# Kernel optimization log

Hardware: AMD Instinct MI355X
Metric: run time of the kernel (lower is better)

## Reference

```python
import jax, jax.numpy as jnp
import numpy as np

B, TX, TY, D, H = 8, 128, 128, 512, 512
LN_EPS = 1e-3  # keras LayerNormalization default epsilon


def setup_inputs() -> dict:
    key = jax.random.key(0)
    ks = jax.random.split(key, 6)
    scale = 1.0 / np.sqrt(D)
    return {
        "context": jax.random.normal(ks[0], (B, TX, D), jnp.float32),
        "x": jax.random.normal(ks[1], (B, TY, D), jnp.float32),
        "Wa": jax.random.normal(ks[2], (D, H), jnp.float32) * scale,
        "bWa": jnp.zeros((H,), jnp.float32),
        "Ua": jax.random.normal(ks[3], (D, H), jnp.float32) * scale,
        "bUa": jnp.zeros((H,), jnp.float32),
        "Va": jax.random.normal(ks[4], (H, 1), jnp.float32) * (1.0 / np.sqrt(H)),
        "bVa": jnp.zeros((1,), jnp.float32),
        "gamma": jnp.ones((D,), jnp.float32),
        "beta": jnp.zeros((D,), jnp.float32),
    }


def reference(context, x, Wa, bWa, Ua, bUa, Va, bVa, gamma, beta):
    # context: [B,Tx,D], x: [B,Ty,D]
    Wc = context @ Wa + bWa                      # [B,Tx,H]
    Ux = x @ Ua + bUa                            # [B,Ty,H]
    t = jnp.tanh(Wc[:, None, :, :] + Ux[:, :, None, :])  # [B,Ty,Tx,H]
    scores = jnp.einsum('btxh,h->btx', t, Va[:, 0]) + bVa[0]  # [B,Ty,Tx]
    attn = jax.nn.softmax(scores, axis=-1)
    cv = jnp.einsum('btx,bxd->btd', attn, context)  # [B,Ty,D]
    mean = jnp.mean(cv, axis=-1, keepdims=True)
    var = jnp.mean(jnp.square(cv - mean), axis=-1, keepdims=True)
    cv = (cv - mean) * jax.lax.rsqrt(var + LN_EPS) * gamma + beta
    return cv + x
```

## Files before the change

### kernel.cpp

```cpp
#include <hip/hip_runtime.h>


#define SCALE 2.8853900817779268f

typedef __attribute__((ext_vector_type(8))) short short8;
typedef float floatx4 __attribute__((ext_vector_type(4)));

__device__ __forceinline__ unsigned short f2bf(float f) {
  union { float f; unsigned u; } c{f};
  unsigned r = (c.u + 0x7FFFu + ((c.u >> 16) & 1u)) >> 16;
  return (unsigned short)r;
}

__global__ __launch_bounds__(512) void gemm_all(
    const float* __restrict__ ctx, const float* __restrict__ xin,
    const float* __restrict__ Wa, const float* __restrict__ Ua,
    const float* __restrict__ bWa, const float* __restrict__ bUa,
    float* __restrict__ WcT, float* __restrict__ Ux) {
  const bool second = (blockIdx.z != 0);
  const float* __restrict__ A = second ? xin : ctx;
  const float* __restrict__ W = second ? Ua : Wa;
  const int m0 = blockIdx.x * 64, n0 = blockIdx.y * 64;

  __shared__ __align__(16) unsigned short As[512 * 8];
  __shared__ __align__(16) unsigned short Bs[512 * 8];

  const int t = threadIdx.x;
  const int lane = t & 63, wv = t >> 6;

  const int skst = t >> 8;
  const int ssub = (t >> 6) & 3;
  const int srow = ssub * 16 + (lane & 15);
  const int sk   = skst * 32 + (lane >> 4) * 8;

  const float* aptr = A + (size_t)(m0 + srow) * 512 + sk;
  const float* wptr = W + (size_t)sk * 512 + n0 + srow;

  const int wrow = wv & 3, wcol = wv >> 2;
  floatx4 acc[2] = {};

  float4 a0 = *(const float4*)(aptr);
  float4 a1 = *(const float4*)(aptr + 4);
  float bw[8];
#pragma unroll
  for (int j = 0; j < 8; j++) bw[j] = wptr[(size_t)j * 512];

  for (int kt = 0; kt < 512; kt += 64) {
    short8 av, bv;
    av[0] = (short)f2bf(a0.x); av[1] = (short)f2bf(a0.y);
    av[2] = (short)f2bf(a0.z); av[3] = (short)f2bf(a0.w);
    av[4] = (short)f2bf(a1.x); av[5] = (short)f2bf(a1.y);
    av[6] = (short)f2bf(a1.z); av[7] = (short)f2bf(a1.w);
#pragma unroll
    for (int j = 0; j < 8; j++) bv[j] = (short)f2bf(bw[j]);
    ((short8*)As)[t] = av;
    ((short8*)Bs)[t] = bv;
    __syncthreads();
    if (kt + 64 < 512) {
      a0 = *(const float4*)(aptr + kt + 64);
      a1 = *(const float4*)(aptr + kt + 68);
      const float* wp2 = wptr + (size_t)(kt + 64) * 512;
#pragma unroll
      for (int j = 0; j < 8; j++) bw[j] = wp2[(size_t)j * 512];
    }
#pragma unroll
    for (int ks = 0; ks < 2; ks++) {
      const short8 af  = ((const short8*)As)[ks * 256 + wrow * 64 + lane];
      const short8 bf0 = ((const short8*)Bs)[ks * 256 + (wcol * 2 + 0) * 64 + lane];
      const short8 bf1 = ((const short8*)Bs)[ks * 256 + (wcol * 2 + 1) * 64 + lane];
      acc[0] = __builtin_amdgcn_mfma_f32_16x16x32_bf16(af, bf0, acc[0], 0, 0, 0);
      acc[1] = __builtin_amdgcn_mfma_f32_16x16x32_bf16(af, bf1, acc[1], 0, 0, 0);
    }
    __syncthreads();
  }

  const int quad = lane >> 4;
  const int mg0 = m0 + wrow * 16 + quad * 4;
  if (!second) {
    const int b = mg0 >> 7, tx0 = mg0 & 127;
#pragma unroll
    for (int i = 0; i < 2; i++) {
      const int h = n0 + wcol * 32 + i * 16 + (lane & 15);
      const float bias = bWa[h] + bUa[h];
      float4 o;
      o.x = (acc[i][0] + bias) * SCALE;
      o.y = (acc[i][1] + bias) * SCALE;
      o.z = (acc[i][2] + bias) * SCALE;
      o.w = (acc[i][3] + bias) * SCALE;
      *(float4*)&WcT[(size_t)b * 65536 + (size_t)h * 128 + tx0] = o;
    }
  } else {
#pragma unroll
    for (int i = 0; i < 2; i++) {
      const int h = n0 + wcol * 32 + i * 16 + (lane & 15);
#pragma unroll
      for (int r = 0; r < 4; r++)
        Ux[(size_t)(mg0 + r) * 512 + h] = acc[i][r] * SCALE;
    }
  }
}

__global__ __launch_bounds__(1024) void attn4(
    const float* __restrict__ WcT, const float* __restrict__ Ux,
    const float* __restrict__ ctx, const float* __restrict__ xin,
    const float* __restrict__ Va,
    const float* __restrict__ gamma, const float* __restrict__ beta,
    float* __restrict__ out) {
  const int b = blockIdx.x >> 5;
  const int ty0 = (blockIdx.x & 31) * 4;
  const int t = threadIdx.x;
  const int lane = t & 63, wv = t >> 6;

  __shared__ __align__(16) float4 s_ux[512];
  __shared__ float s_va[512];
  __shared__ float s_part[32][128];
  __shared__ __align__(16) float4 s_at[128];
  __shared__ float s_red[4][2][8];
  __shared__ float s_mv[4][2];

  {
    const float* uxb = Ux + (size_t)(b * 128 + ty0) * 512;
    for (int i = t; i < 2048; i += 1024) {
      const int r = i >> 9, h = i & 511;
      ((float*)&s_ux[h])[r] = uxb[i];
    }
    if (t < 512) s_va[t] = Va[t];
  }
  __syncthreads();

  const int tx = t & 127, hq = t >> 7;
  {
    const float* wp = WcT + (size_t)b * 65536 + (size_t)hq * 8192 + tx;
    float a0 = 0.f, a1 = 0.f, a2 = 0.f, a3 = 0.f;
#pragma unroll 4
    for (int hh = 0; hh < 64; hh++) {
      const float w = wp[(size_t)hh * 128];
      const float4 u = s_ux[hq * 64 + hh];
      const float va = s_va[hq * 64 + hh];
      a0 = fmaf(va, __builtin_amdgcn_rcpf(1.0f + __builtin_amdgcn_exp2f(w + u.x)), a0);
      a1 = fmaf(va, __builtin_amdgcn_rcpf(1.0f + __builtin_amdgcn_exp2f(w + u.y)), a1);
      a2 = fmaf(va, __builtin_amdgcn_rcpf(1.0f + __builtin_amdgcn_exp2f(w + u.z)), a2);
      a3 = fmaf(va, __builtin_amdgcn_rcpf(1.0f + __builtin_amdgcn_exp2f(w + u.w)), a3);
    }
    s_part[hq * 4 + 0][tx] = a0;
    s_part[hq * 4 + 1][tx] = a1;
    s_part[hq * 4 + 2][tx] = a2;
    s_part[hq * 4 + 3][tx] = a3;
  }
  __syncthreads();

  if (wv < 4) {
    const int r = wv;
    float sA = 0.f, sB = 0.f;
#pragma unroll
    for (int q = 0; q < 8; q++) {
      sA += s_part[q * 4 + r][lane];
      sB += s_part[q * 4 + r][lane + 64];
    }
    sA *= -2.0f; sB *= -2.0f;
    float m = fmaxf(sA, sB);
#pragma unroll
    for (int off = 32; off; off >>= 1) m = fmaxf(m, __shfl_xor(m, off));
    const float eA = __expf(sA - m);
    const float eB = __expf(sB - m);
    float sm = eA + eB;
#pragma unroll
    for (int off = 32; off; off >>= 1) sm += __shfl_xor(sm, off);
    const float inv = __builtin_amdgcn_rcpf(sm);
    ((float*)&s_at[lane])[r] = eA * inv;
    ((float*)&s_at[lane + 64])[r] = eB * inv;
  }
  __syncthreads();

  float cv[4] = {0.f, 0.f, 0.f, 0.f};
  if (t < 512) {
    const float* cp = ctx + (size_t)b * 65536 + t;
#pragma unroll 4
    for (int x = 0; x < 128; x++) {
      const float c = cp[(size_t)x * 512];
      const float4 at = s_at[x];
      cv[0] = fmaf(at.x, c, cv[0]);
      cv[1] = fmaf(at.y, c, cv[1]);
      cv[2] = fmaf(at.z, c, cv[2]);
      cv[3] = fmaf(at.w, c, cv[3]);
    }
#pragma unroll
    for (int r = 0; r < 4; r++) {
      float sm = cv[r], q = cv[r] * cv[r];
#pragma unroll
      for (int off = 32; off; off >>= 1) {
        sm += __shfl_xor(sm, off);
        q += __shfl_xor(q, off);
      }
      if (lane == 0) { s_red[r][0][wv] = sm; s_red[r][1][wv] = q; }
    }
  }
  __syncthreads();
  if (t < 4) {
    float sm = 0.f, q = 0.f;
#pragma unroll
    for (int i = 0; i < 8; i++) { sm += s_red[t][0][i]; q += s_red[t][1][i]; }
    const float mean = sm * (1.0f / 512.0f);
    const float var = q * (1.0f / 512.0f) - mean * mean;
    s_mv[t][0] = mean;
    s_mv[t][1] = __builtin_amdgcn_rsqf(var + 1e-3f);
  }
  __syncthreads();

  if (t < 512) {
    const float g = gamma[t], bb = beta[t];
#pragma unroll
    for (int r = 0; r < 4; r++) {
      const int row = b * 128 + ty0 + r;
      const float xv = xin[(size_t)row * 512 + t];
      out[(size_t)row * 512 + t] = (cv[r] - s_mv[r][0]) * s_mv[r][1] * g + bb + xv;
    }
  }
}

extern "C" void kernel_launch(void* const* d_in, const int* in_sizes, int n_in,
                              void* d_out, int out_size, void* d_ws, size_t ws_size,
                              hipStream_t stream) {
  const float* ctx   = (const float*)d_in[0];
  const float* xin   = (const float*)d_in[1];
  const float* Wa    = (const float*)d_in[2];
  const float* bWa   = (const float*)d_in[3];
  const float* Ua    = (const float*)d_in[4];
  const float* bUa   = (const float*)d_in[5];
  const float* Va    = (const float*)d_in[6];
  const float* gamma = (const float*)d_in[8];
  const float* beta  = (const float*)d_in[9];
  float* out = (float*)d_out;

  char* ws = (char*)d_ws;
  float* WcT = (float*)ws;
  float* Ux  = (float*)(ws + (2u << 20));

  gemm_all<<<dim3(16, 8, 2), 512, 0, stream>>>(ctx, xin, Wa, Ua, bWa, bUa, WcT, Ux);
  attn4<<<256, 1024, 0, stream>>>(WcT, Ux, ctx, xin, Va, gamma, beta, out);
}
```

Baseline: 109.2 us.

## Retile projection GEMM, truncate bf16 via perm, spread context sum over all threads

The projection GEMM now uses 32-row tiles with a 128-deep K step, which doubles the grid to 512 blocks and halves the number of K iterations per block. Its bf16 conversion switches from round-to-nearest to truncation packed with a single perm instruction. In the attention kernel, the context-vector accumulation and layernorm stage now runs on all 1024 threads, each covering two rows instead of four, rather than leaving half the block idle. Risks are slightly lower accuracy from truncation and the context matrix being loaded twice per block.

```diff
diff --git a/kernel.cpp b/kernel.cpp
--- a/kernel.cpp
+++ b/kernel.cpp
@@ -6,10 +6,9 @@
 typedef __attribute__((ext_vector_type(8))) short short8;
 typedef float floatx4 __attribute__((ext_vector_type(4)));
 
-__device__ __forceinline__ unsigned short f2bf(float f) {
-  union { float f; unsigned u; } c{f};
-  unsigned r = (c.u + 0x7FFFu + ((c.u >> 16) & 1u)) >> 16;
-  return (unsigned short)r;
+__device__ __forceinline__ unsigned pack_bf_trunc(float lo, float hi) {
+  return __builtin_amdgcn_perm(__float_as_uint(hi), __float_as_uint(lo),
+                               0x07060302u);
 }
 
 __global__ __launch_bounds__(512) void gemm_all(
@@ -20,83 +19,92 @@
   const bool second = (blockIdx.z != 0);
   const float* __restrict__ A = second ? xin : ctx;
   const float* __restrict__ W = second ? Ua : Wa;
-  const int m0 = blockIdx.x * 64, n0 = blockIdx.y * 64;
+  const int m0 = blockIdx.x * 32, n0 = blockIdx.y * 64;
 
   __shared__ __align__(16) unsigned short As[512 * 8];
-  __shared__ __align__(16) unsigned short Bs[512 * 8];
+  __shared__ __align__(16) unsigned short Bs[1024 * 8];
 
   const int t = threadIdx.x;
   const int lane = t & 63, wv = t >> 6;
 
-  const int skst = t >> 8;
-  const int ssub = (t >> 6) & 3;
-  const int srow = ssub * 16 + (lane & 15);
-  const int sk   = skst * 32 + (lane >> 4) * 8;
-
-  const float* aptr = A + (size_t)(m0 + srow) * 512 + sk;
-  const float* wptr = W + (size_t)sk * 512 + n0 + srow;
-
-  const int wrow = wv & 3, wcol = wv >> 2;
-  floatx4 acc[2] = {};
+  const int arow = ((t >> 6) & 1) * 16 + (t & 15);
+  const int ak   = (t >> 7) * 32 + ((t & 63) >> 4) * 8;
+  const float* aptr = A + (size_t)(m0 + arow) * 512 + ak;
+
+  const int bn0_ = ((t >> 6) & 3) * 16 + (t & 15);
+  const int bk0_ = (t >> 8) * 32 + ((t & 63) >> 4) * 8;
+  const int s2 = t + 512;
+  const int bn1_ = ((s2 >> 6) & 3) * 16 + (s2 & 15);
+  const int bk1_ = (s2 >> 8) * 32 + ((s2 & 63) >> 4) * 8;
+  const float* bptr0 = W + (size_t)bk0_ * 512 + n0 + bn0_;
+  const float* bptr1 = W + (size_t)bk1_ * 512 + n0 + bn1_;
+
+  const int wm = wv & 1, wn = wv >> 1;
+  floatx4 acc = {};
 
   float4 a0 = *(const float4*)(aptr);
   float4 a1 = *(const float4*)(aptr + 4);
-  float bw[8];
-#pragma unroll
-  for (int j = 0; j < 8; j++) bw[j] = wptr[(size_t)j * 512];
-
-  for (int kt = 0; kt < 512; kt += 64) {
-    short8 av, bv;
-    av[0] = (short)f2bf(a0.x); av[1] = (short)f2bf(a0.y);
-    av[2] = (short)f2bf(a0.z); av[3] = (short)f2bf(a0.w);
-    av[4] = (short)f2bf(a1.x); av[5] = (short)f2bf(a1.y);
-    av[6] = (short)f2bf(a1.z); av[7] = (short)f2bf(a1.w);
-#pragma unroll
-    for (int j = 0; j < 8; j++) bv[j] = (short)f2bf(bw[j]);
-    ((short8*)As)[t] = av;
-    ((short8*)Bs)[t] = bv;
+  float bw0[8], bw1[8];
+#pragma unroll
+  for (int j = 0; j < 8; j++) {
+    bw0[j] = bptr0[(size_t)j * 512];
+    bw1[j] = bptr1[(size_t)j * 512];
+  }
+
+  for (int kt = 0; kt < 512; kt += 128) {
+    union { short8 s; uint4 u; } av, bv0, bv1;
+    av.u.x = pack_bf_trunc(a0.x, a0.y);
+    av.u.y = pack_bf_trunc(a0.z, a0.w);
+    av.u.z = pack_bf_trunc(a1.x, a1.y);
+    av.u.w = pack_bf_trunc(a1.z, a1.w);
+    bv0.u.x = pack_bf_trunc(bw0[0], bw0[1]);
+    bv0.u.y = pack_bf_trunc(bw0[2], bw0[3]);
+    bv0.u.z = pack_bf_trunc(bw0[4], bw0[5]);
+    bv0.u.w = pack_bf_trunc(bw0[6], bw0[7]);
+    bv1.u.x = pack_bf_trunc(bw1[0], bw1[1]);
+    bv1.u.y = pack_bf_trunc(bw1[2], bw1[3]);
+    bv1.u.z = pack_bf_trunc(bw1[4], bw1[5]);
+    bv1.u.w = pack_bf_trunc(bw1[6], bw1[7]);
+    ((short8*)As)[t] = av.s;
+    ((short8*)Bs)[t] = bv0.s;
+    ((short8*)Bs)[t + 512] = bv1.s;
     __syncthreads();
-    if (kt + 64 < 512) {
-      a0 = *(const float4*)(aptr + kt + 64);
-      a1 = *(const float4*)(aptr + kt + 68);
-      const float* wp2 = wptr + (size_t)(kt + 64) * 512;
-#pragma unroll
-      for (int j = 0; j < 8; j++) bw[j] = wp2[(size_t)j * 512];
-    }
-#pragma unroll
-    for (int ks = 0; ks < 2; ks++) {
-      const short8 af  = ((const short8*)As)[ks * 256 + wrow * 64 + lane];
-      const short8 bf0 = ((const short8*)Bs)[ks * 256 + (wcol * 2 + 0) * 64 + lane];
-      const short8 bf1 = ((const short8*)Bs)[ks * 256 + (wcol * 2 + 1) * 64 + lane];
-      acc[0] = __builtin_amdgcn_mfma_f32_16x16x32_bf16(af, bf0, acc[0], 0, 0, 0);
-      acc[1] = __builtin_amdgcn_mfma_f32_16x16x32_bf16(af, bf1, acc[1], 0, 0, 0);
+    if (kt + 128 < 512) {
+      a0 = *(const float4*)(aptr + kt + 128);
+      a1 = *(const float4*)(aptr + kt + 132);
+      const float* p0 = bptr0 + (size_t)(kt + 128) * 512;
+      const float* p1 = bptr1 + (size_t)(kt + 128) * 512;
+#pragma unroll
+      for (int j = 0; j < 8; j++) {
+        bw0[j] = p0[(size_t)j * 512];
+        bw1[j] = p1[(size_t)j * 512];
+      }
+    }
+#pragma unroll
+    for (int ks = 0; ks < 4; ks++) {
+      const short8 af = ((const short8*)As)[ks * 128 + wm * 64 + lane];
+      const short8 bf = ((const short8*)Bs)[ks * 256 + wn * 64 + lane];
+      acc = __builtin_amdgcn_mfma_f32_16x16x32_bf16(af, bf, acc, 0, 0, 0);
     }
     __syncthreads();
   }
 
   const int quad = lane >> 4;
-  const int mg0 = m0 + wrow * 16 + quad * 4;
+  const int h = n0 + wn * 16 + (lane & 15);
+  const int mg0 = m0 + wm * 16 + quad * 4;
   if (!second) {
+    const float bias = bWa[h] + bUa[h];
     const int b = mg0 >> 7, tx0 = mg0 & 127;
-#pragma unroll
-    for (int i = 0; i < 2; i++) {
-      const int h = n0 + wcol * 32 + i * 16 + (lane & 15);
-      const float bias = bWa[h] + bUa[h];
-      float4 o;
-      o.x = (acc[i][0] + bias) * SCALE;
-      o.y = (acc[i][1] + bias) * SCALE;
-      o.z = (acc[i][2] + bias) * SCALE;
-      o.w = (acc[i][3] + bias) * SCALE;
-      *(float4*)&WcT[(size_t)b * 65536 + (size_t)h * 128 + tx0] = o;
-    }
+    float4 o;
+    o.x = (acc[0] + bias) * SCALE;
+    o.y = (acc[1] + bias) * SCALE;
+    o.z = (acc[2] + bias) * SCALE;
+    o.w = (acc[3] + bias) * SCALE;
+    *(float4*)&WcT[(size_t)b * 65536 + (size_t)h * 128 + tx0] = o;
   } else {
 #pragma unroll
-    for (int i = 0; i < 2; i++) {
-      const int h = n0 + wcol * 32 + i * 16 + (lane & 15);
-#pragma unroll
-      for (int r = 0; r < 4; r++)
-        Ux[(size_t)(mg0 + r) * 512 + h] = acc[i][r] * SCALE;
-    }
+    for (int r = 0; r < 4; r++)
+      Ux[(size_t)(mg0 + r) * 512 + h] = acc[r] * SCALE;
   }
 }
 
@@ -172,27 +180,32 @@
   }
   __syncthreads();
 
-  float cv[4] = {0.f, 0.f, 0.f, 0.f};
-  if (t < 512) {
-    const float* cp = ctx + (size_t)b * 65536 + t;
+  const int d = t & 511, rh = t >> 9;
+  float cv0 = 0.f, cv1 = 0.f;
+  {
+    const float* cp = ctx + (size_t)b * 65536 + d;
 #pragma unroll 4
     for (int x = 0; x < 128; x++) {
       const float c = cp[(size_t)x * 512];
-      const float4 at = s_at[x];
-      cv[0] = fmaf(at.x, c, cv[0]);
-      cv[1] = fmaf(at.y, c, cv[1]);
-      cv[2] = fmaf(at.z, c, cv[2]);
-      cv[3] = fmaf(at.w, c, cv[3]);
-    }
-#pragma unroll
-    for (int r = 0; r < 4; r++) {
-      float sm = cv[r], q = cv[r] * cv[r];
-#pragma unroll
-      for (int off = 32; off; off >>= 1) {
-        sm += __shfl_xor(sm, off);
-        q += __shfl_xor(q, off);
-      }
-      if (lane == 0) { s_red[r][0][wv] = sm; s_red[r][1][wv] = q; }
+      const float2 at = *(const float2*)((const float*)&s_at[x] + rh * 2);
+      cv0 = fmaf(at.x, c, cv0);
+      cv1 = fmaf(at.y, c, cv1);
+    }
+  }
+
+  const int wh = wv & 7;
+#pragma unroll
+  for (int j = 0; j < 2; j++) {
+    const float v = j ? cv1 : cv0;
+    float sm = v, q = v * v;
+#pragma unroll
+    for (int off = 32; off; off >>= 1) {
+      sm += __shfl_xor(sm, off);
+      q += __shfl_xor(q, off);
+    }
+    if (lane == 0) {
+      s_red[rh * 2 + j][0][wh] = sm;
+      s_red[rh * 2 + j][1][wh] = q;
     }
   }
   __syncthreads();
@@ -207,13 +220,15 @@
   }
   __syncthreads();
 
-  if (t < 512) {
-    const float g = gamma[t], bb = beta[t];
-#pragma unroll
-    for (int r = 0; r < 4; r++) {
+  {
+    const float g = gamma[d], bb = beta[d];
+#pragma unroll
+    for (int j = 0; j < 2; j++) {
+      const int r = rh * 2 + j;
       const int row = b * 128 + ty0 + r;
-      const float xv = xin[(size_t)row * 512 + t];
-      out[(size_t)row * 512 + t] = (cv[r] - s_mv[r][0]) * s_mv[r][1] * g + bb + xv;
+      const float v = j ? cv1 : cv0;
+      const float xv = xin[(size_t)row * 512 + d];
+      out[(size_t)row * 512 + d] = (v - s_mv[r][0]) * s_mv[r][1] * g + bb + xv;
     }
   }
 }
@@ -236,6 +251,6 @@
   float* WcT = (float*)ws;
   float* Ux  = (float*)(ws + (2u << 20));
 
-  gemm_all<<<dim3(16, 8, 2), 512, 0, stream>>>(ctx, xin, Wa, Ua, bWa, bUa, WcT, Ux);
+  gemm_all<<<dim3(32, 8, 2), 512, 0, stream>>>(ctx, xin, Wa, Ua, bWa, bUa, WcT, Ux);
   attn4<<<256, 1024, 0, stream>>>(WcT, Ux, ctx, xin, Va, gamma, beta, out);
 }
```

Result: no change. 108.3 us (-0.8%).
